# Kernel tuning notes

Measured on AMD Instinct MI355X. Metric: run time of the kernel, lower is better.

The kernel has to match this reference:

```python
import jax, jax.numpy as jnp
import numpy as np

B, SR, D, H, L, NH, ND, E, RK = 64, 29, 768, 3072, 12, 12, 14, 15, 8
S = SR + 1            # cls token + regions
SCALE = 16.0 / 8.0    # lora_alpha / lora_r
NE = L // 2           # number of even (MoE) layers


def _ln(x, g, b, eps):
    m = x.mean(-1, keepdims=True)
    v = ((x - m) ** 2).mean(-1, keepdims=True)
    return (x - m) * jax.lax.rsqrt(v + eps) * g + b


def _ln_plain(x, eps):
    # F.layer_norm with no affine params (expert output norm)
    m = x.mean(-1, keepdims=True)
    v = ((x - m) ** 2).mean(-1, keepdims=True)
    return (x - m) * jax.lax.rsqrt(v + eps)


def _mha(x, Wq, bq, Wk, bk, Wv, bv, Wo, bo):
    b_, s_, _ = x.shape
    dh = D // NH
    q = (x @ Wq.T + bq).reshape(b_, s_, NH, dh)
    k = (x @ Wk.T + bk).reshape(b_, s_, NH, dh)
    v = (x @ Wv.T + bv).reshape(b_, s_, NH, dh)
    att = jax.nn.softmax(jnp.einsum('bqhd,bkhd->bhqk', q, k) / np.float32(np.sqrt(dh)), axis=-1)
    o = jnp.einsum('bhqk,bkhd->bqhd', att, v).reshape(b_, s_, D)
    return o @ Wo.T + bo


def _forward(region_features, mask, cls_token, ln1_g, ln1_b, ln2_g, ln2_b,
             Wq, bq, Wk, bk, Wv, bv, Wao, bao, Wi, bi, Wo, bo, fg, fb,
             cW1, cb1, clng, clnb, cW2, cb2, A_up, B_up, A_down, B_down):
    bsz = region_features.shape[0]
    h = jnp.concatenate([jnp.broadcast_to(cls_token, (bsz, 1, D)), region_features], axis=1)
    col_counts = mask.sum(axis=0)  # [ND], guaranteed > 0 by construction
    for i in range(L):
        n1 = _ln(h, ln1_g[i], ln1_b[i], 1e-12)
        attn = _mha(n1, Wq[i], bq[i], Wk[i], bk[i], Wv[i], bv[i], Wao[i], bao[i])
        res1 = attn + h
        n2 = _ln(res1, ln2_g[i], ln2_b[i], 1e-12)
        inter = jax.nn.gelu(n2 @ Wi[i].T + bi[i], approximate=False)   # [B,S,H]
        base = inter @ Wo[i].T + bo[i]                                  # [B,S,D]
        if i % 2 == 0:
            e = i // 2
            # disease classifier: mask-gather region attention features, mean-pool, per-disease MLP
            region = attn[:, 1:, :]                                     # [B,SR,D]
            pooled = jnp.einsum('rd,brh->bdh', mask, region) / col_counts[None, :, None]
            z = jnp.einsum('bdh,dkh->bdk', pooled, cW1[e]) + cb1[e]
            z = jax.nn.gelu(_ln(z, clng[e], clnb[e], 1e-5), approximate=False)
            preds = jnp.einsum('bdk,dk->bd', z, cW2[e]) + cb2[e]        # [B,ND]
            disease_active = (jax.nn.sigmoid(preds) > 0.5).astype(h.dtype)
            # expert activation: general expert always on; disease experts per region-disease mask
            active = jnp.zeros((bsz, S, E), h.dtype).at[:, :, -1].set(1.0)
            region_active = disease_active[:, None, :] * mask[None, :, :]  # [B,SR,ND]
            active = active.at[:, 1:1 + SR, :ND].set(region_active)
            weights = active / jnp.maximum(active.sum(-1, keepdims=True), 1.0)
            # all 15 LoRA experts densely; zero-weight experts contribute nothing
            lup = jnp.einsum('bser,ehr->bseh', jnp.einsum('bsd,erd->bser', n2, A_up[e]), B_up[e]) * SCALE
            hid = inter[:, :, None, :] + lup                             # [B,S,E,H]
            ldown = jnp.einsum('bser,edr->bsed', jnp.einsum('bseh,erh->bser', hid, A_down[e]), B_down[e]) * SCALE
            out_e = _ln_plain(base[:, :, None, :] + ldown, 1e-5)         # [B,S,E,D]
            ffn_out = jnp.einsum('bsed,bse->bsd', out_e, weights)
        else:
            ffn_out = base
        h = ffn_out + res1
    return _ln(h, fg, fb, 1e-12)


def setup_inputs() -> dict:
    key = jax.random.key(0)
    ks = iter(jax.random.split(key, 64))
    p = lambda *sh: 0.02 * jax.random.normal(next(ks), sh, dtype=jnp.float32)
    g = lambda *sh: 1.0 + 0.02 * jax.random.normal(next(ks), sh, dtype=jnp.float32)
    return dict(
        region_features=jax.random.normal(next(ks), (B, SR, D), dtype=jnp.float32),
        mask=jax.random.bernoulli(next(ks), 0.5, (SR, ND)).astype(jnp.float32).at[0, :].set(1.0),
        cls_token=p(1, 1, D),
        ln1_g=g(L, D), ln1_b=p(L, D), ln2_g=g(L, D), ln2_b=p(L, D),
        Wq=p(L, D, D), bq=p(L, D), Wk=p(L, D, D), bk=p(L, D),
        Wv=p(L, D, D), bv=p(L, D), Wao=p(L, D, D), bao=p(L, D),
        Wi=p(L, H, D), bi=p(L, H), Wo=p(L, D, H), bo=p(L, D),
        fg=g(D), fb=p(D),
        cW1=p(NE, ND, D // 2, D), cb1=p(NE, ND, D // 2),
        clng=g(NE, ND, D // 2), clnb=p(NE, ND, D // 2),
        cW2=p(NE, ND, D // 2), cb2=p(NE, ND),
        A_up=p(NE, E, RK, D), B_up=p(NE, E, H, RK),
        A_down=p(NE, E, RK, H), B_down=p(NE, E, D, RK),
    )


def reference(region_features, mask, cls_token, ln1_g, ln1_b, ln2_g, ln2_b,
              Wq, bq, Wk, bk, Wv, bv, Wao, bao, Wi, bi, Wo, bo, fg, fb,
              cW1, cb1, clng, clnb, cW2, cb2, A_up, B_up, A_down, B_down):
    return _forward(region_features, mask, cls_token, ln1_g, ln1_b, ln2_g, ln2_b,
                    Wq, bq, Wk, bk, Wv, bv, Wao, bao, Wi, bi, Wo, bo, fg, fb,
                    cW1, cb1, clng, clnb, cW2, cb2, A_up, B_up, A_down, B_down)
```

## Files before the change

kernel.cpp:

```cpp
#include <hip/hip_runtime.h>

namespace {

constexpr int kB = 64, kSR = 29, kS = 30, kD = 768, kH = 3072, kL = 12;
constexpr int kNH = 12, kND = 14, kE = 15, kNE = 6;
constexpr int kRows = kB * kS;
constexpr int kQKV = 2304;
constexpr long kPS = (long)kRows * kD;
constexpr long kPSL = (long)kRows * 128;

typedef __attribute__((ext_vector_type(8))) short s16x8;
typedef __attribute__((ext_vector_type(4))) float fx4;

__device__ __forceinline__ float gelu_f(float x) {
  return 0.5f * x * (1.0f + erff(x * 0.70710678118654752f));
}

__device__ __forceinline__ unsigned short f2bf_u(float x) {
  union { float f; unsigned u; } v;
  v.f = x;
  unsigned r = v.u + 0x7fffu + ((v.u >> 16) & 1u);
  return (unsigned short)(r >> 16);
}
__device__ __forceinline__ float bfu2f(unsigned short h) {
  union { unsigned u; float f; } v;
  v.u = ((unsigned)h) << 16;
  return v.f;
}

__device__ __forceinline__ void g2l16(const short* g, short* l) {
  __builtin_amdgcn_global_load_lds(
      (const __attribute__((address_space(1))) unsigned int*)g,
      (__attribute__((address_space(3))) unsigned int*)l, 16, 0, 0);
}

template <int N>
__device__ __forceinline__ void waitcnt_vm() {
  if constexpr (N == 0)
    asm volatile("s_waitcnt vmcnt(0)" ::: "memory");
  else if constexpr (N == 4)
    asm volatile("s_waitcnt vmcnt(4)" ::: "memory");
  else if constexpr (N == 6)
    asm volatile("s_waitcnt vmcnt(6)" ::: "memory");
  else
    asm volatile("s_waitcnt vmcnt(8)" ::: "memory");
  __builtin_amdgcn_sched_barrier(0);
}

__device__ __forceinline__ void swz_block(int& bx, int& by, int& bz) {
  int gx = gridDim.x, gy = gridDim.y;
  int nwg = gx * gy * (int)gridDim.z;
  int orig = blockIdx.x + gx * (blockIdx.y + gy * blockIdx.z);
  int q = nwg >> 3, r = nwg & 7;
  int xcd = orig & 7, idx = orig >> 3;
  int s = (xcd < r ? xcd * (q + 1) : r * (q + 1) + (xcd - r) * q) + idx;
  bx = s % gx;
  int t2 = s / gx;
  by = t2 % gy;
  bz = t2 / gy;
}

__device__ __forceinline__ float block_sum(float v) {
  __shared__ float sb[4];
#pragma unroll
  for (int o = 32; o > 0; o >>= 1) v += __shfl_down(v, o, 64);
  int w = threadIdx.x >> 6;
  __syncthreads();
  if ((threadIdx.x & 63) == 0) sb[w] = v;
  __syncthreads();
  return sb[0] + sb[1] + sb[2] + sb[3];
}

__device__ __forceinline__ float dot8(const float* __restrict__ p,
                                      const float* __restrict__ q) {
  float4 x = *(const float4*)p;
  float4 y = *(const float4*)(p + 4);
  return x.x * q[0] + x.y * q[1] + x.z * q[2] + x.w * q[3] +
         y.x * q[4] + y.y * q[5] + y.z * q[6] + y.w * q[7];
}

template <int BM, int BN, int MODE>
__global__ __launch_bounds__(256) void gemm_hl(
    const short* __restrict__ Ah, const short* __restrict__ Al,
    const short* __restrict__ Bh, const short* __restrict__ Bl,
    const float* __restrict__ bias, float* __restrict__ Cf,
    short* __restrict__ Ch, short* __restrict__ Cl, int K, int ldc, int act,
    int kchunk, long bsA, long bsB, long bsBias, long bsC) {
  constexpr int MFR = BM / 16, NFR = BN / 16;
  constexpr int NA = 2 * MFR, NB = 2 * NFR, LPW = (NA + NB) / 4;
  constexpr int MF_W = MFR / 2, NF_W = NFR / 2;
  constexpr int ABUF = 2 * MFR * 512, BBUF = 2 * NFR * 512;
  __shared__ __align__(16) short As[3][2][MFR][512];
  __shared__ __align__(16) short Bs[3][2][NFR][512];
  int bx, by, bz;
  swz_block(bx, by, bz);
  const int t = threadIdx.x, w = t >> 6, lane = t & 63;
  const int lr = lane & 15, lg = lane >> 4;
  const int m0 = by * BM, n0 = bx * BN;
  const int kst = K >> 5;
  int k0 = 0;
  if (MODE == 1) {
    k0 = bz * kchunk;
    Cf += bz * bsC;
  }
  if (MODE == 2) {
    Ah += bz * bsA;
    Al += bz * bsA;
    Bh += bz * bsB;
    Bl += bz * bsB;
    if (bias) bias += bz * bsBias;
    Cf += bz * bsC;
  }
  const int nsteps = (MODE == 1 ? kchunk : K) >> 5;
  const int wmf = (w & 1) * MF_W, wnf = (w >> 1) * NF_W;

  const short* gp[LPW];
  short* lp[LPW];
  int bo[LPW], adv[LPW];
#pragma unroll
  for (int q = 0; q < LPW; q++) {
    int f = w * LPW + q;
    if (f < NA) {
      int p = f & 1, mf = f >> 1;
      gp[q] = (p ? Al : Ah) + (size_t)(m0 + mf * 16 + lr) * K + k0 + lg * 8;
      lp[q] = &As[0][p][mf][0];
      bo[q] = ABUF;
      adv[q] = 32;
    } else {
      int fb = f - NA, p = fb & 1, nf = fb >> 1;
      gp[q] = (p ? Bl : Bh) + ((size_t)(n0 / 16 + nf) * kst + (k0 >> 5)) * 512 +
              lane * 8;
      lp[q] = &Bs[0][p][nf][0];
      bo[q] = BBUF;
      adv[q] = 512;
    }
  }

  auto stage = [&](int bufidx) {
#pragma unroll
    for (int q = 0; q < LPW; q++) {
      g2l16(gp[q], lp[q] + bufidx * bo[q]);
      gp[q] += adv[q];
    }
  };

  fx4 acc[MF_W][NF_W];
#pragma unroll
  for (int i = 0; i < MF_W; i++)
#pragma unroll
    for (int j = 0; j < NF_W; j++) acc[i][j] = (fx4)0.f;

  stage(0);
  stage(1);
  waitcnt_vm<LPW>();
  __builtin_amdgcn_s_barrier();
  __builtin_amdgcn_sched_barrier(0);

  int cur = 0;
  for (int s = 0; s < nsteps; s++) {
    if (s + 2 < nsteps) {
      int nb = cur + 2;
      if (nb >= 3) nb -= 3;
      stage(nb);
    }
    s16x8 af[MF_W][2], bf[NF_W][2];
#pragma unroll
    for (int fm = 0; fm < MF_W; fm++) {
      af[fm][0] = *(const s16x8*)&As[cur][0][wmf + fm][lane * 8];
      af[fm][1] = *(const s16x8*)&As[cur][1][wmf + fm][lane * 8];
    }
#pragma unroll
    for (int fn = 0; fn < NF_W; fn++) {
      bf[fn][0] = *(const s16x8*)&Bs[cur][0][wnf + fn][lane * 8];
      bf[fn][1] = *(const s16x8*)&Bs[cur][1][wnf + fn][lane * 8];
    }
#pragma unroll
    for (int fm = 0; fm < MF_W; fm++)
#pragma unroll
      for (int fn = 0; fn < NF_W; fn++)
        acc[fm][fn] = __builtin_amdgcn_mfma_f32_16x16x32_bf16(
            af[fm][0], bf[fn][0], acc[fm][fn], 0, 0, 0);
#pragma unroll
    for (int fm = 0; fm < MF_W; fm++)
#pragma unroll
      for (int fn = 0; fn < NF_W; fn++)
        acc[fm][fn] = __builtin_amdgcn_mfma_f32_16x16x32_bf16(
            af[fm][0], bf[fn][1], acc[fm][fn], 0, 0, 0);
#pragma unroll
    for (int fm = 0; fm < MF_W; fm++)
#pragma unroll
      for (int fn = 0; fn < NF_W; fn++)
        acc[fm][fn] = __builtin_amdgcn_mfma_f32_16x16x32_bf16(
            af[fm][1], bf[fn][0], acc[fm][fn], 0, 0, 0);
    if (s + 2 < nsteps)
      waitcnt_vm<LPW>();
    else
      waitcnt_vm<0>();
    __builtin_amdgcn_s_barrier();
    __builtin_amdgcn_sched_barrier(0);
    cur = (cur == 2) ? 0 : cur + 1;
  }

  const int orow = (lane >> 4) * 4;
#pragma unroll
  for (int fm = 0; fm < MF_W; fm++) {
#pragma unroll
    for (int fn = 0; fn < NF_W; fn++) {
      int col = n0 + (wnf + fn) * 16 + lr;
      if (MODE == 1) {
#pragma unroll
        for (int j = 0; j < 4; j++) {
          int row = m0 + (wmf + fm) * 16 + orow + j;
          Cf[(size_t)row * ldc + col] = acc[fm][fn][j];
        }
      } else {
        float bv = bias ? bias[col] : 0.f;
#pragma unroll
        for (int j = 0; j < 4; j++) {
          int row = m0 + (wmf + fm) * 16 + orow + j;
          float v = acc[fm][fn][j] + bv;
          if (act) v = gelu_f(v);
          size_t idx = (size_t)row * ldc + col;
          if (Cf) Cf[idx] = v;
          if (Ch) {
            unsigned short hb = f2bf_u(v);
            Ch[idx] = (short)hb;
            Cl[idx] = (short)f2bf_u(v - bfu2f(hb));
          }
        }
      }
    }
  }
}

__device__ __forceinline__ void pack_store(const float* src, short* ph,
                                           short* pl, size_t o) {
  float4 a = *(const float4*)src;
  float4 b = *(const float4*)(src + 4);
  float v[8] = {a.x, a.y, a.z, a.w, b.x, b.y, b.z, b.w};
  s16x8 hv, lv;
#pragma unroll
  for (int e = 0; e < 8; e++) {
    unsigned short h = f2bf_u(v[e]);
    hv[e] = (short)h;
    lv[e] = (short)f2bf_u(v[e] - bfu2f(h));
  }
  *(s16x8*)(ph + o) = hv;
  *(s16x8*)(pl + o) = lv;
}

__global__ __launch_bounds__(256) void pack_layer_k(
    const float* __restrict__ Wq, const float* __restrict__ Wk,
    const float* __restrict__ Wv, const float* __restrict__ Wao,
    const float* __restrict__ Wi, const float* __restrict__ Wo,
    short* __restrict__ qph, short* __restrict__ qpl, short* __restrict__ aph,
    short* __restrict__ apl, short* __restrict__ iph, short* __restrict__ ipl,
    short* __restrict__ oph, short* __restrict__ opl) {
  int tile = blockIdx.x * 4 + (threadIdx.x >> 6);
  int lane = threadIdx.x & 63;
  int lr = lane & 15, lg = lane >> 4;
  const float* src;
  short *ph, *pl;
  size_t o;
  if (tile < 3456) {
    int nf = tile / 24, ks = tile % 24;
    int row = nf * 16 + lr;
    const float* W = row < 768 ? Wq : row < 1536 ? Wk : Wv;
    int r = row < 768 ? row : row < 1536 ? row - 768 : row - 1536;
    src = W + (size_t)r * 768 + ks * 32 + lg * 8;
    ph = qph; pl = qpl;
    o = (size_t)tile * 512 + lane * 8;
  } else if (tile < 4608) {
    int idx = tile - 3456;
    int nf = idx / 24, ks = idx % 24;
    src = Wao + (size_t)(nf * 16 + lr) * 768 + ks * 32 + lg * 8;
    ph = aph; pl = apl;
    o = (size_t)idx * 512 + lane * 8;
  } else if (tile < 9216) {
    int idx = tile - 4608;
    int nf = idx / 24, ks = idx % 24;
    src = Wi + (size_t)(nf * 16 + lr) * 768 + ks * 32 + lg * 8;
    ph = iph; pl = ipl;
    o = (size_t)idx * 512 + lane * 8;
  } else {
    int idx = tile - 9216;
    int nf = idx / 96, ks = idx % 96;
    src = Wo + (size_t)(nf * 16 + lr) * 3072 + ks * 32 + lg * 8;
    ph = oph; pl = opl;
    o = (size_t)idx * 512 + lane * 8;
  }
  pack_store(src, ph, pl, o);
}

__global__ __launch_bounds__(256) void pack_w_k(const float* __restrict__ W,
                                                short* __restrict__ ph,
                                                short* __restrict__ pl, int K,
                                                int ntiles) {
  int tile = blockIdx.x * 4 + (threadIdx.x >> 6);
  if (tile >= ntiles) return;
  int kst = K >> 5;
  int nf = tile / kst, ks = tile - nf * kst;
  int lane = threadIdx.x & 63;
// ... 80 lines not shown
  for (int c = 0; c < 3; c++) {
    int tt = t + c * 256;
    float dd = (c == 0 ? d0 : c == 1 ? d1 : d2);
    float val = dd * inv * g[tt] + b[tt];
    unsigned short hb = f2bf_u(val);
    yh[rb + tt] = (short)hb;
    yl[rb + tt] = (short)f2bf_u(val - bfu2f(hb));
  }
}

__global__ __launch_bounds__(256) void ln_parts_k(
    const float* __restrict__ parts, const float* __restrict__ b2,
    const float* __restrict__ r2, float* __restrict__ hout,
    const float* __restrict__ g, const float* __restrict__ b,
    short* __restrict__ yh, short* __restrict__ yl, float eps) {
  int row = blockIdx.x;
  int t = threadIdx.x;
  long rb = (long)row * kD;
  float v0, v1, v2;
  {
    float s0 = 0, s1 = 0, s2 = 0;
#pragma unroll
    for (int p = 0; p < 4; p++) {
      s0 += parts[p * kPS + rb + t];
      s1 += parts[p * kPS + rb + t + 256];
      s2 += parts[p * kPS + rb + t + 512];
    }
    v0 = s0 + b2[t] + r2[rb + t];
    v1 = s1 + b2[t + 256] + r2[rb + t + 256];
    v2 = s2 + b2[t + 512] + r2[rb + t + 512];
  }
  hout[rb + t] = v0;
  hout[rb + t + 256] = v1;
  hout[rb + t + 512] = v2;
  float m = block_sum(v0 + v1 + v2) * (1.0f / 768.0f);
  float d0 = v0 - m, d1 = v1 - m, d2 = v2 - m;
  float q = block_sum(d0 * d0 + d1 * d1 + d2 * d2);
  float inv = rsqrtf(q * (1.0f / 768.0f) + eps);
#pragma unroll
  for (int c = 0; c < 3; c++) {
    int tt = t + c * 256;
    float dd = (c == 0 ? d0 : c == 1 ? d1 : d2);
    float val = dd * inv * g[tt] + b[tt];
    unsigned short hb = f2bf_u(val);
    yh[rb + tt] = (short)hb;
    yl[rb + tt] = (short)f2bf_u(val - bfu2f(hb));
  }
}

__global__ __launch_bounds__(256) void ln_row_k(
    const float* __restrict__ parts, const float* __restrict__ b2,
    const float* __restrict__ r2, const float* __restrict__ g,
    const float* __restrict__ b, float* __restrict__ y, float eps) {
  int row = blockIdx.x;
  int t = threadIdx.x;
  long rb = (long)row * kD;
  float s0 = 0, s1 = 0, s2 = 0;
#pragma unroll
  for (int p = 0; p < 4; p++) {
    s0 += parts[p * kPS + rb + t];
    s1 += parts[p * kPS + rb + t + 256];
    s2 += parts[p * kPS + rb + t + 512];
  }
  float v0 = s0 + b2[t] + r2[rb + t];
  float v1 = s1 + b2[t + 256] + r2[rb + t + 256];
  float v2 = s2 + b2[t + 512] + r2[rb + t + 512];
  float m = block_sum(v0 + v1 + v2) * (1.0f / 768.0f);
  float d0 = v0 - m, d1 = v1 - m, d2 = v2 - m;
  float q = block_sum(d0 * d0 + d1 * d1 + d2 * d2);
  float inv = rsqrtf(q * (1.0f / 768.0f) + eps);
  y[rb + t] = d0 * inv * g[t] + b[t];
  y[rb + t + 256] = d1 * inv * g[t + 256] + b[t + 256];
  y[rb + t + 512] = d2 * inv * g[t + 512] + b[t + 512];
}

__global__ __launch_bounds__(256) void addln_bf_k(
    const float* __restrict__ aparts, const float* __restrict__ abias,
    const float* __restrict__ hh, const float* __restrict__ g,
    const float* __restrict__ b, float* __restrict__ r1,
    short* __restrict__ n2h, short* __restrict__ n2l, float eps) {
  int row = blockIdx.x;
  int t = threadIdx.x;
  long rb = (long)row * kD;
  float v0 = aparts[rb + t] + aparts[kPS + rb + t] + abias[t] + hh[rb + t];
  float v1 = aparts[rb + t + 256] + aparts[kPS + rb + t + 256] + abias[t + 256] +
             hh[rb + t + 256];
  float v2 = aparts[rb + t + 512] + aparts[kPS + rb + t + 512] + abias[t + 512] +
             hh[rb + t + 512];
  r1[rb + t] = v0;
  r1[rb + t + 256] = v1;
  r1[rb + t + 512] = v2;
  float m = block_sum(v0 + v1 + v2) * (1.0f / 768.0f);
  float d0 = v0 - m, d1 = v1 - m, d2 = v2 - m;
  float q = block_sum(d0 * d0 + d1 * d1 + d2 * d2);
  float inv = rsqrtf(q * (1.0f / 768.0f) + eps);
#pragma unroll
  for (int c = 0; c < 3; c++) {
    int tt = t + c * 256;
    float dd = (c == 0 ? d0 : c == 1 ? d1 : d2);
    float val = dd * inv * g[tt] + b[tt];
    unsigned short hb = f2bf_u(val);
    n2h[rb + tt] = (short)hb;
    n2l[rb + tt] = (short)f2bf_u(val - bfu2f(hb));
  }
}

__global__ __launch_bounds__(256) void attn_k(const float* __restrict__ qkv,
                                              const float* __restrict__ bq,
                                              const float* __restrict__ bk,
                                              const float* __restrict__ bv,
                                              short* __restrict__ oh,
                                              short* __restrict__ ol) {
  int blk = blockIdx.x;
  int b = blk / kNH, hh = blk % kNH;
  __shared__ float qs[30][65], ks[30][65], vs[30][65], ps[30][32];
  int t = threadIdx.x;
  long ibase = (long)b * kS * kQKV + hh * 64;
  long obase = (long)b * kS * kD + hh * 64;
  for (int idx = t; idx < 1920; idx += 256) {
    int s = idx >> 6, d = idx & 63;
    long a = ibase + (long)s * kQKV + d;
    int bcol = hh * 64 + d;
    qs[s][d] = qkv[a] + bq[bcol];
    ks[s][d] = qkv[a + 768] + bk[bcol];
    vs[s][d] = qkv[a + 1536] + bv[bcol];
  }
  __syncthreads();
  for (int idx = t; idx < 900; idx += 256) {
    int r = idx / 30, c = idx % 30;
    float acc = 0.f;
#pragma unroll
    for (int d = 0; d < 64; d++) acc += qs[r][d] * ks[c][d];
    ps[r][c] = acc * 0.125f;
  }
  __syncthreads();
  if (t < 30) {
    float mx = -1e30f;
#pragma unroll
    for (int c = 0; c < 30; c++) mx = fmaxf(mx, ps[t][c]);
    float sm = 0.f;
#pragma unroll
    for (int c = 0; c < 30; c++) sm += expf(ps[t][c] - mx);
    float inv = 1.0f / sm;
#pragma unroll
    for (int c = 0; c < 30; c++) ps[t][c] = expf(ps[t][c] - mx) * inv;
  }
  __syncthreads();
  for (int idx = t; idx < 1920; idx += 256) {
    int r = idx >> 6, d = idx & 63;
    float acc = 0.f;
#pragma unroll
    for (int c = 0; c < 30; c++) acc += ps[r][c] * vs[c][d];
    long a = obase + (long)r * kD + d;
    unsigned short hb = f2bf_u(acc);
    oh[a] = (short)hb;
    ol[a] = (short)f2bf_u(acc - bfu2f(hb));
  }
}

__global__ __launch_bounds__(256) void pool_k(const float* __restrict__ aparts,
                                              const float* __restrict__ bao,
                                              const float* __restrict__ mask,
                                              const float* __restrict__ cc,
                                              short* __restrict__ ph,
                                              short* __restrict__ pl) {
  int blk = blockIdx.x;
  int d = blk >> 6, b = blk & 63;
  __shared__ float mr[32];
  int t = threadIdx.x;
  if (t < kSR) mr[t] = mask[t * kND + d];
  __syncthreads();
  float inv = 1.0f / cc[d];
  for (int hd = t; hd < kD; hd += 256) {
    float acc = 0.f;
    for (int r = 0; r < kSR; r++) {
      long o = ((long)b * kS + 1 + r) * kD + hd;
      acc += mr[r] * (aparts[o] + aparts[kPS + o]);
    }
    float v = acc * inv + bao[hd];
    unsigned short hb = f2bf_u(v);
    size_t o = (size_t)blk * kD + hd;
    ph[o] = (short)hb;
    pl[o] = (short)f2bf_u(v - bfu2f(hb));
  }
}

__global__ __launch_bounds__(256) void cls2_k(const float* __restrict__ z,
                                              const float* __restrict__ lng,
                                              const float* __restrict__ lnb,
                                              const float* __restrict__ w2,
                                              const float* __restrict__ b2,
                                              float* __restrict__ da) {
  int blk = blockIdx.x;
  int d = blk >> 6, b = blk & 63;
  int t = threadIdx.x;
  const float* zr = z + (long)blk * 384;
  float v0 = zr[t];
  float v1 = (t < 128) ? zr[256 + t] : 0.f;
  float m = block_sum(v0 + v1) * (1.0f / 384.0f);
  float d0 = v0 - m;
  float d1 = (t < 128) ? v1 - m : 0.f;
  float q = block_sum(d0 * d0 + d1 * d1);
  float inv = rsqrtf(q * (1.0f / 384.0f) + 1e-5f);
  const float* lg = lng + (long)d * 384;
  const float* lb = lnb + (long)d * 384;
  const float* wd = w2 + (long)d * 384;
  float p = gelu_f(d0 * inv * lg[t] + lb[t]) * wd[t];
  if (t < 128) p += gelu_f(d1 * inv * lg[256 + t] + lb[256 + t]) * wd[256 + t];
  float ps = block_sum(p);
  if (t == 0) da[b * kND + d] = (ps + b2[d] > 0.f) ? 1.f : 0.f;
}

__global__ __launch_bounds__(256) void vcomb_k(const float* __restrict__ ubp,
                                               const float* __restrict__ iap,
                                               const float* __restrict__ Mm,
                                               float* __restrict__ vv) {
  int idx = blockIdx.x * 256 + threadIdx.x;
  if (idx >= kRows * 120) return;
  int row = idx / 120, c = idx % 120;
  int e = c >> 3, rp = c & 7;
  const float* Me = Mm + e * 64 + rp * 8;
  long rb = (long)row * 128;
  float acc = 0.f;
#pragma unroll
  for (int p = 0; p < 8; p++) acc += iap[p * kPSL + rb + c];
  float uv[8];
#pragma unroll
  for (int r = 0; r < 8; r++) {
    float u = 0.f;
#pragma unroll
    for (int p = 0; p < 4; p++) u += ubp[p * kPSL + rb + e * 8 + r];
    uv[r] = u;
  }
#pragma unroll
  for (int r = 0; r < 8; r++) acc += 2.0f * Me[r] * uv[r];
  vv[rb + c] = acc;
}

__global__ __launch_bounds__(256) void finaleven_k(
    const float* __restrict__ parts, const float* __restrict__ bo,
    const float* __restrict__ res1, const float* __restrict__ vv,
    const float* __restrict__ Bd, const float* __restrict__ da,
    const float* __restrict__ mask, float* __restrict__ h,
    const float* __restrict__ g1, const float* __restrict__ b1,
    short* __restrict__ n1h, short* __restrict__ n1l) {
  int row = blockIdx.x;
  int b = row / kS, s = row % kS;
  int t = threadIdx.x;
  __shared__ float w[16];
  __shared__ float vvs[120];
  if (t < 120) vvs[t] = vv[(long)row * 128 + t];
  if (t < kND) w[t] = (s >= 1) ? da[b * kND + t] * mask[(s - 1) * kND + t] : 0.f;
  if (t == kND) w[kND] = 1.f;
  __syncthreads();
  float wsum = 0.f;
#pragma unroll
  for (int e = 0; e < kE; e++) wsum += w[e];
  float winv = 1.0f / wsum;
  long rb = (long)row * kD;
  float b0 = bo[t], b1v = bo[t + 256], b2v = bo[t + 512];
#pragma unroll
  for (int p = 0; p < 4; p++) {
    b0 += parts[p * kPS + rb + t];
    b1v += parts[p * kPS + rb + t + 256];
    b2v += parts[p * kPS + rb + t + 512];
  }
  float a0 = 0.f, a1 = 0.f, a2 = 0.f;
  for (int e = 0; e < kE; e++) {
    float we = w[e];
    if (we == 0.f) continue;
    const float* vr = vvs + e * 8;
    float y0 = b0 + 2.0f * dot8(Bd + ((long)(e * kD + t)) * 8, vr);
    float y1 = b1v + 2.0f * dot8(Bd + ((long)(e * kD + t + 256)) * 8, vr);
    float y2 = b2v + 2.0f * dot8(Bd + ((long)(e * kD + t + 512)) * 8, vr);
    float m = block_sum(y0 + y1 + y2) * (1.0f / 768.0f);
    float d0 = y0 - m, d1 = y1 - m, d2 = y2 - m;
    float q = block_sum(d0 * d0 + d1 * d1 + d2 * d2);
    float inv = rsqrtf(q * (1.0f / 768.0f) + 1e-5f);
    float sc = we * winv * inv;
    a0 += sc * d0;
    a1 += sc * d1;
    a2 += sc * d2;
  }
  float v0 = a0 + res1[rb + t];
  float v1 = a1 + res1[rb + t + 256];
  float v2 = a2 + res1[rb + t + 512];
  h[rb + t] = v0;
  h[rb + t + 256] = v1;
  h[rb + t + 512] = v2;
  float m = block_sum(v0 + v1 + v2) * (1.0f / 768.0f);
  float d0 = v0 - m, d1 = v1 - m, d2 = v2 - m;
  float q = block_sum(d0 * d0 + d1 * d1 + d2 * d2);
  float inv = rsqrtf(q * (1.0f / 768.0f) + 1e-12f);
#pragma unroll
  for (int c = 0; c < 3; c++) {
    int tt = t + c * 256;
    float dd = (c == 0 ? d0 : c == 1 ? d1 : d2);
    float val = dd * inv * g1[tt] + b1[tt];
    unsigned short hb = f2bf_u(val);
    n1h[rb + tt] = (short)hb;
    n1l[rb + tt] = (short)f2bf_u(val - bfu2f(hb));
  }
}

}

extern "C" void kernel_launch(void* const* d_in, const int* in_sizes, int n_in,
                              void* d_out, int out_size, void* d_ws, size_t ws_size,
                              hipStream_t stream) {
  const float* region = (const float*)d_in[0];
  const float* mask = (const float*)d_in[1];
  const float* cls = (const float*)d_in[2];
  const float* ln1g = (const float*)d_in[3];
  const float* ln1b = (const float*)d_in[4];
  const float* ln2g = (const float*)d_in[5];
  const float* ln2b = (const float*)d_in[6];
  const float* Wq = (const float*)d_in[7];
  const float* bq = (const float*)d_in[8];
  const float* Wk = (const float*)d_in[9];
  const float* bk = (const float*)d_in[10];
  const float* Wv = (const float*)d_in[11];
  const float* bv = (const float*)d_in[12];
  const float* Wao = (const float*)d_in[13];
  const float* bao = (const float*)d_in[14];
  const float* Wi = (const float*)d_in[15];
  const float* bi = (const float*)d_in[16];
  const float* Wo = (const float*)d_in[17];
  const float* bo = (const float*)d_in[18];
  const float* fg = (const float*)d_in[19];
  const float* fb = (const float*)d_in[20];
  const float* cW1 = (const float*)d_in[21];
  const float* cb1 = (const float*)d_in[22];
  const float* clng = (const float*)d_in[23];
  const float* clnb = (const float*)d_in[24];
  const float* cW2 = (const float*)d_in[25];
  const float* cb2 = (const float*)d_in[26];
  const float* Aup = (const float*)d_in[27];
  const float* Bup = (const float*)d_in[28];
  const float* Adn = (const float*)d_in[29];
  const float* Bdn = (const float*)d_in[30];
  float* out = (float*)d_out;

  char* wsb = (char*)d_ws;
  size_t off = 0;
  auto alloc = [&](size_t bytes) {
    char* p = wsb + off;
    off = (off + bytes + 255) & ~(size_t)255;
    return (void*)p;
  };
  float* h = (float*)alloc((size_t)kRows * kD * 4);
  float* qkv = (float*)alloc((size_t)kRows * kQKV * 4);
  float* aop = (float*)alloc((size_t)2 * kRows * kD * 4);
  float* res1 = (float*)alloc((size_t)kRows * kD * 4);
  float* cwop = (float*)alloc((size_t)4 * kRows * kD * 4);
  float* zb = (float*)alloc((size_t)kND * kB * 384 * 4);
  float* da = (float*)alloc((size_t)kB * kND * 4);
  float* ubp = (float*)alloc((size_t)4 * kRows * 128 * 4);
  float* iap = (float*)alloc((size_t)8 * kRows * 128 * 4);
  float* vvb = (float*)alloc((size_t)kRows * 128 * 4);
  float* Mm = (float*)alloc((size_t)kNE * kE * 64 * 4);
  float* cc = (float*)alloc(64);
  short* n1h = (short*)alloc((size_t)kRows * kD * 2);
  short* n1l = (short*)alloc((size_t)kRows * kD * 2);
  short* n2h = (short*)alloc((size_t)kRows * kD * 2);
  short* n2l = (short*)alloc((size_t)kRows * kD * 2);
  short* inth = (short*)alloc((size_t)kRows * kH * 2);
  short* intl = (short*)alloc((size_t)kRows * kH * 2);
  short* pooledh = (short*)alloc((size_t)kND * kB * kD * 2);
  short* pooledl = (short*)alloc((size_t)kND * kB * kD * 2);
  short* qkvph = (short*)alloc((size_t)144 * 24 * 512 * 2);
  short* qkvpl = (short*)alloc((size_t)144 * 24 * 512 * 2);
  short* waoph = (short*)alloc((size_t)48 * 24 * 512 * 2);
  short* waopl = (short*)alloc((size_t)48 * 24 * 512 * 2);
  short* wiph = (short*)alloc((size_t)192 * 24 * 512 * 2);
  short* wipl = (short*)alloc((size_t)192 * 24 * 512 * 2);
  short* woph = (short*)alloc((size_t)48 * 96 * 512 * 2);
  short* wopl = (short*)alloc((size_t)48 * 96 * 512 * 2);
  short* luph = (short*)alloc((size_t)8 * 24 * 512 * 2);
  short* lupl = (short*)alloc((size_t)8 * 24 * 512 * 2);
  short* ldph = (short*)alloc((size_t)8 * 96 * 512 * 2);
  short* ldpl = (short*)alloc((size_t)8 * 96 * 512 * 2);
  short* cw1ph = (short*)alloc((size_t)336 * 24 * 512 * 2);
  short* cw1pl = (short*)alloc((size_t)336 * 24 * 512 * 2);

  concat_k<<<(kRows * kD + 255) / 256, 256, 0, stream>>>(region, cls, h);
  cc_k<<<1, 32, 0, stream>>>(mask, cc);
  mmat_k<<<kNE * kE, 256, 0, stream>>>(Adn, Bup, Mm);

  const int nDD = kD * kD;
  const int nDH = kD * kH;

  ln_bf_k<<<kRows, 256, 0, stream>>>(h, ln1g, ln1b, n1h, n1l, 1e-12f);

  for (int i = 0; i < kL; i++) {
    int le = i >> 1;
    bool even = (i % 2) == 0;
    pack_layer_k<<<3456, 256, 0, stream>>>(
        Wq + (long)i * nDD, Wk + (long)i * nDD, Wv + (long)i * nDD,
        Wao + (long)i * nDD, Wi + (long)i * nDH, Wo + (long)i * nDH, qkvph,
        qkvpl, waoph, waopl, wiph, wipl, woph, wopl);

    gemm_hl<128, 128, 0><<<dim3(18, 15), 256, 0, stream>>>(
        n1h, n1l, qkvph, qkvpl, nullptr, qkv, nullptr, nullptr, 768, kQKV, 0, 0,
        0, 0, 0, 0);
    attn_k<<<kB * kNH, 256, 0, stream>>>(qkv, bq + i * kD, bk + i * kD,
                                         bv + i * kD, n1h, n1l);
    gemm_hl<128, 128, 1><<<dim3(6, 15, 2), 256, 0, stream>>>(
        n1h, n1l, waoph, waopl, nullptr, aop, nullptr, nullptr, 768, kD, 0, 384,
        0, 0, 0, kPS);
    addln_bf_k<<<kRows, 256, 0, stream>>>(aop, bao + i * kD, h, ln2g + i * kD,
                                          ln2b + i * kD, res1, n2h, n2l, 1e-12f);
    gemm_hl<128, 128, 0><<<dim3(24, 15), 256, 0, stream>>>(
        n2h, n2l, wiph, wipl, bi + i * kH, nullptr, inth, intl, 768, kH, 1, 0,
        0, 0, 0, 0);
    gemm_hl<128, 128, 1><<<dim3(6, 15, 4), 256, 0, stream>>>(
        inth, intl, woph, wopl, nullptr, cwop, nullptr, nullptr, 3072, kD, 0,
        768, 0, 0, 0, kPS);
    if (even) {
      pack_pad_k<<<48, 256, 0, stream>>>(Aup + (long)le * kE * 8 * kD, luph,
                                         lupl, 768);
      pack_pad_k<<<192, 256, 0, stream>>>(Adn + (long)le * kE * 8 * kH, ldph,
                                          ldpl, 3072);
      pack_w_k<<<(336 * 24) / 4, 256, 0, stream>>>(
          cW1 + (long)le * kND * 384 * kD, cw1ph, cw1pl, 768, 336 * 24);
      gemm_hl<128, 128, 1><<<dim3(1, 15, 4), 256, 0, stream>>>(
          n2h, n2l, luph, lupl, nullptr, ubp, nullptr, nullptr, 768, 128, 0, 192,
          0, 0, 0, kPSL);
      gemm_hl<128, 128, 1><<<dim3(1, 15, 8), 256, 0, stream>>>(
          inth, intl, ldph, ldpl, nullptr, iap, nullptr, nullptr, 3072, 128, 0,
          384, 0, 0, 0, kPSL);
      pool_k<<<kND * kB, 256, 0, stream>>>(aop, bao + i * kD, mask, cc, pooledh,
                                           pooledl);
      gemm_hl<64, 64, 2><<<dim3(6, 1, 14), 256, 0, stream>>>(
          pooledh, pooledl, cw1ph, cw1pl, cb1 + (long)le * kND * 384, zb,
          nullptr, nullptr, 768, 384, 0, 0, (long)64 * kD, (long)576 * 512, 384,
          (long)64 * 384);
      cls2_k<<<kND * kB, 256, 0, stream>>>(zb, clng + (long)le * kND * 384,
                                           clnb + (long)le * kND * 384,
                                           cW2 + (long)le * kND * 384,
                                           cb2 + le * kND, da);
      vcomb_k<<<(kRows * 120 + 255) / 256, 256, 0, stream>>>(
          ubp, iap, Mm + le * kE * 64, vvb);
      finaleven_k<<<kRows, 256, 0, stream>>>(
          cwop, bo + i * kD, res1, vvb, Bdn + (long)le * kE * kD * 8, da, mask,
          h, ln1g + (i + 1) * kD, ln1b + (i + 1) * kD, n1h, n1l);
    } else if (i < kL - 1) {
      ln_parts_k<<<kRows, 256, 0, stream>>>(cwop, bo + i * kD, res1, h,
                                            ln1g + (i + 1) * kD,
                                            ln1b + (i + 1) * kD, n1h, n1l,
                                            1e-12f);
    } else {
      ln_row_k<<<kRows, 256, 0, stream>>>(cwop, bo + i * kD, res1, fg, fb, out,
                                          1e-12f);
    }
  }
}
```

Before: 3.269 ms.

## Replace LDS-staged GEMM with register double-buffered direct-global GEMM

The triple-buffered LDS pipeline (global_load_lds plus barriers) is replaced by a kernel where each wave loads its own 64x64 tile fragments straight from global memory into registers, ping-ponging two register sets. This removes LDS traffic and block-wide barriers. In exchange, operands that waves could share through LDS are now fetched separately, raising global/L2 traffic and register pressure. The classifier GEMM grid is halved and rows beyond M are skipped.

```diff
diff --git a/kernel.cpp b/kernel.cpp
--- a/kernel.cpp
+++ b/kernel.cpp
@@ -26,25 +26,6 @@
   union { unsigned u; float f; } v;
   v.u = ((unsigned)h) << 16;
   return v.f;
-}
-
-__device__ __forceinline__ void g2l16(const short* g, short* l) {
-  __builtin_amdgcn_global_load_lds(
-      (const __attribute__((address_space(1))) unsigned int*)g,
-      (__attribute__((address_space(3))) unsigned int*)l, 16, 0, 0);
-}
-
-template <int N>
-__device__ __forceinline__ void waitcnt_vm() {
-  if constexpr (N == 0)
-    asm volatile("s_waitcnt vmcnt(0)" ::: "memory");
-  else if constexpr (N == 4)
-    asm volatile("s_waitcnt vmcnt(4)" ::: "memory");
-  else if constexpr (N == 6)
-    asm volatile("s_waitcnt vmcnt(6)" ::: "memory");
-  else
-    asm volatile("s_waitcnt vmcnt(8)" ::: "memory");
-  __builtin_amdgcn_sched_barrier(0);
 }
 
 __device__ __forceinline__ void swz_block(int& bx, int& by, int& bz) {
@@ -79,24 +60,17 @@
          y.x * q[4] + y.y * q[5] + y.z * q[6] + y.w * q[7];
 }
 
-template <int BM, int BN, int MODE>
-__global__ __launch_bounds__(256) void gemm_hl(
+template <int MODE>
+__global__ __launch_bounds__(256) void gemm_reg(
     const short* __restrict__ Ah, const short* __restrict__ Al,
     const short* __restrict__ Bh, const short* __restrict__ Bl,
     const float* __restrict__ bias, float* __restrict__ Cf,
     short* __restrict__ Ch, short* __restrict__ Cl, int K, int ldc, int act,
-    int kchunk, long bsA, long bsB, long bsBias, long bsC) {
-  constexpr int MFR = BM / 16, NFR = BN / 16;
-  constexpr int NA = 2 * MFR, NB = 2 * NFR, LPW = (NA + NB) / 4;
-  constexpr int MF_W = MFR / 2, NF_W = NFR / 2;
-  constexpr int ABUF = 2 * MFR * 512, BBUF = 2 * NFR * 512;
-  __shared__ __align__(16) short As[3][2][MFR][512];
-  __shared__ __align__(16) short Bs[3][2][NFR][512];
+    int kchunk, long bsA, long bsB, long bsBias, long bsC, int M) {
   int bx, by, bz;
   swz_block(bx, by, bz);
   const int t = threadIdx.x, w = t >> 6, lane = t & 63;
   const int lr = lane & 15, lg = lane >> 4;
-  const int m0 = by * BM, n0 = bx * BN;
   const int kst = K >> 5;
   int k0 = 0;
   if (MODE == 1) {
@@ -111,113 +85,112 @@
     if (bias) bias += bz * bsBias;
     Cf += bz * bsC;
   }
+  const int m0 = by * 128 + (w & 1) * 64;
+  const int n0 = bx * 128 + (w >> 1) * 64;
+  if (MODE == 2 && m0 >= M) return;
   const int nsteps = (MODE == 1 ? kchunk : K) >> 5;
-  const int wmf = (w & 1) * MF_W, wnf = (w >> 1) * NF_W;
-
-  const short* gp[LPW];
-  short* lp[LPW];
-  int bo[LPW], adv[LPW];
-#pragma unroll
-  for (int q = 0; q < LPW; q++) {
-    int f = w * LPW + q;
-    if (f < NA) {
-      int p = f & 1, mf = f >> 1;
-      gp[q] = (p ? Al : Ah) + (size_t)(m0 + mf * 16 + lr) * K + k0 + lg * 8;
-      lp[q] = &As[0][p][mf][0];
-      bo[q] = ABUF;
-      adv[q] = 32;
-    } else {
-      int fb = f - NA, p = fb & 1, nf = fb >> 1;
-      gp[q] = (p ? Bl : Bh) + ((size_t)(n0 / 16 + nf) * kst + (k0 >> 5)) * 512 +
-              lane * 8;
-      lp[q] = &Bs[0][p][nf][0];
-      bo[q] = BBUF;
-      adv[q] = 512;
+
+  const short* ga[4][2];
+  const short* gb[4][2];
+#pragma unroll
+  for (int mf = 0; mf < 4; mf++) {
+    size_t ro = (size_t)(m0 + mf * 16 + lr) * K + k0 + lg * 8;
+    ga[mf][0] = Ah + ro;
+    ga[mf][1] = Al + ro;
+  }
+#pragma unroll
+  for (int nf = 0; nf < 4; nf++) {
+    size_t to = ((size_t)(n0 / 16 + nf) * kst + (k0 >> 5)) * 512 + lane * 8;
+    gb[nf][0] = Bh + to;
+    gb[nf][1] = Bl + to;
+  }
+
+  fx4 acc[4][4];
+#pragma unroll
+  for (int i = 0; i < 4; i++)
+#pragma unroll
+    for (int j = 0; j < 4; j++) acc[i][j] = (fx4)0.f;
+
+  s16x8 a0[4][2], b0[4][2], a1[4][2], b1[4][2];
+
+  auto load0 = [&]() {
+#pragma unroll
+    for (int mf = 0; mf < 4; mf++) {
+      a0[mf][0] = *(const s16x8*)ga[mf][0];
+      a0[mf][1] = *(const s16x8*)ga[mf][1];
+      ga[mf][0] += 32;
+      ga[mf][1] += 32;
     }
-  }
-
-  auto stage = [&](int bufidx) {
-#pragma unroll
-    for (int q = 0; q < LPW; q++) {
-      g2l16(gp[q], lp[q] + bufidx * bo[q]);
-      gp[q] += adv[q];
+#pragma unroll
+    for (int nf = 0; nf < 4; nf++) {
+      b0[nf][0] = *(const s16x8*)gb[nf][0];
+      b0[nf][1] = *(const s16x8*)gb[nf][1];
+      gb[nf][0] += 512;
+      gb[nf][1] += 512;
     }
   };
-
-  fx4 acc[MF_W][NF_W];
-#pragma unroll
-  for (int i = 0; i < MF_W; i++)
-#pragma unroll
-    for (int j = 0; j < NF_W; j++) acc[i][j] = (fx4)0.f;
-
-  stage(0);
-  stage(1);
-  waitcnt_vm<LPW>();
-  __builtin_amdgcn_s_barrier();
-  __builtin_amdgcn_sched_barrier(0);
-
-  int cur = 0;
-  for (int s = 0; s < nsteps; s++) {
-    if (s + 2 < nsteps) {
-      int nb = cur + 2;
-      if (nb >= 3) nb -= 3;
-      stage(nb);
+  auto load1 = [&]() {
+#pragma unroll
+    for (int mf = 0; mf < 4; mf++) {
+      a1[mf][0] = *(const s16x8*)ga[mf][0];
+      a1[mf][1] = *(const s16x8*)ga[mf][1];
+      ga[mf][0] += 32;
+      ga[mf][1] += 32;
     }
-    s16x8 af[MF_W][2], bf[NF_W][2];
-#pragma unroll
-    for (int fm = 0; fm < MF_W; fm++) {
-      af[fm][0] = *(const s16x8*)&As[cur][0][wmf + fm][lane * 8];
-      af[fm][1] = *(const s16x8*)&As[cur][1][wmf + fm][lane * 8];
+#pragma unroll
+    for (int nf = 0; nf < 4; nf++) {
+      b1[nf][0] = *(const s16x8*)gb[nf][0];
+      b1[nf][1] = *(const s16x8*)gb[nf][1];
+      gb[nf][0] += 512;
+      gb[nf][1] += 512;
     }
-#pragma unroll
-    for (int fn = 0; fn < NF_W; fn++) {
-      bf[fn][0] = *(const s16x8*)&Bs[cur][0][wnf + fn][lane * 8];
-      bf[fn][1] = *(const s16x8*)&Bs[cur][1][wnf + fn][lane * 8];
-    }
-#pragma unroll
-    for (int fm = 0; fm < MF_W; fm++)
-#pragma unroll
-      for (int fn = 0; fn < NF_W; fn++)
+  };
+  auto mfma3 = [&](s16x8 (&a)[4][2], s16x8 (&b)[4][2]) {
+#pragma unroll
+    for (int fm = 0; fm < 4; fm++)
+#pragma unroll
+      for (int fn = 0; fn < 4; fn++)
         acc[fm][fn] = __builtin_amdgcn_mfma_f32_16x16x32_bf16(
-            af[fm][0], bf[fn][0], acc[fm][fn], 0, 0, 0);
-#pragma unroll
-    for (int fm = 0; fm < MF_W; fm++)
-#pragma unroll
-      for (int fn = 0; fn < NF_W; fn++)
+            a[fm][0], b[fn][0], acc[fm][fn], 0, 0, 0);
+#pragma unroll
+    for (int fm = 0; fm < 4; fm++)
+#pragma unroll
+      for (int fn = 0; fn < 4; fn++)
         acc[fm][fn] = __builtin_amdgcn_mfma_f32_16x16x32_bf16(
-            af[fm][0], bf[fn][1], acc[fm][fn], 0, 0, 0);
-#pragma unroll
-    for (int fm = 0; fm < MF_W; fm++)
-#pragma unroll
-      for (int fn = 0; fn < NF_W; fn++)
+            a[fm][0], b[fn][1], acc[fm][fn], 0, 0, 0);
+#pragma unroll
+    for (int fm = 0; fm < 4; fm++)
+#pragma unroll
+      for (int fn = 0; fn < 4; fn++)
         acc[fm][fn] = __builtin_amdgcn_mfma_f32_16x16x32_bf16(
-            af[fm][1], bf[fn][0], acc[fm][fn], 0, 0, 0);
-    if (s + 2 < nsteps)
-      waitcnt_vm<LPW>();
-    else
-      waitcnt_vm<0>();
-    __builtin_amdgcn_s_barrier();
-    __builtin_amdgcn_sched_barrier(0);
-    cur = (cur == 2) ? 0 : cur + 1;
+            a[fm][1], b[fn][0], acc[fm][fn], 0, 0, 0);
+  };
+
+  load0();
+  for (int s = 0; s < nsteps; s += 2) {
+    load1();
+    mfma3(a0, b0);
+    if (s + 2 < nsteps) load0();
+    mfma3(a1, b1);
   }
 
   const int orow = (lane >> 4) * 4;
 #pragma unroll
-  for (int fm = 0; fm < MF_W; fm++) {
-#pragma unroll
-    for (int fn = 0; fn < NF_W; fn++) {
-      int col = n0 + (wnf + fn) * 16 + lr;
+  for (int fm = 0; fm < 4; fm++) {
+#pragma unroll
+    for (int fn = 0; fn < 4; fn++) {
+      int col = n0 + fn * 16 + lr;
       if (MODE == 1) {
 #pragma unroll
         for (int j = 0; j < 4; j++) {
-          int row = m0 + (wmf + fm) * 16 + orow + j;
+          int row = m0 + fm * 16 + orow + j;
           Cf[(size_t)row * ldc + col] = acc[fm][fn][j];
         }
       } else {
         float bv = bias ? bias[col] : 0.f;
 #pragma unroll
         for (int j = 0; j < 4; j++) {
-          int row = m0 + (wmf + fm) * 16 + orow + j;
+          int row = m0 + fm * 16 + orow + j;
           float v = acc[fm][fn][j] + bv;
           if (act) v = gelu_f(v);
           size_t idx = (size_t)row * ldc + col;
@@ -782,22 +755,22 @@
         Wao + (long)i * nDD, Wi + (long)i * nDH, Wo + (long)i * nDH, qkvph,
         qkvpl, waoph, waopl, wiph, wipl, woph, wopl);
 
-    gemm_hl<128, 128, 0><<<dim3(18, 15), 256, 0, stream>>>(
+    gemm_reg<0><<<dim3(18, 15), 256, 0, stream>>>(
         n1h, n1l, qkvph, qkvpl, nullptr, qkv, nullptr, nullptr, 768, kQKV, 0, 0,
-        0, 0, 0, 0);
+        0, 0, 0, 0, 0);
     attn_k<<<kB * kNH, 256, 0, stream>>>(qkv, bq + i * kD, bk + i * kD,
                                          bv + i * kD, n1h, n1l);
-    gemm_hl<128, 128, 1><<<dim3(6, 15, 2), 256, 0, stream>>>(
+    gemm_reg<1><<<dim3(6, 15, 2), 256, 0, stream>>>(
         n1h, n1l, waoph, waopl, nullptr, aop, nullptr, nullptr, 768, kD, 0, 384,
-        0, 0, 0, kPS);
+        0, 0, 0, kPS, 0);
     addln_bf_k<<<kRows, 256, 0, stream>>>(aop, bao + i * kD, h, ln2g + i * kD,
                                           ln2b + i * kD, res1, n2h, n2l, 1e-12f);
-    gemm_hl<128, 128, 0><<<dim3(24, 15), 256, 0, stream>>>(
+    gemm_reg<0><<<dim3(24, 15), 256, 0, stream>>>(
         n2h, n2l, wiph, wipl, bi + i * kH, nullptr, inth, intl, 768, kH, 1, 0,
-        0, 0, 0, 0);
-    gemm_hl<128, 128, 1><<<dim3(6, 15, 4), 256, 0, stream>>>(
+        0, 0, 0, 0, 0);
+    gemm_reg<1><<<dim3(6, 15, 4), 256, 0, stream>>>(
         inth, intl, woph, wopl, nullptr, cwop, nullptr, nullptr, 3072, kD, 0,
-        768, 0, 0, 0, kPS);
+        768, 0, 0, 0, kPS, 0);
     if (even) {
       pack_pad_k<<<48, 256, 0, stream>>>(Aup + (long)le * kE * 8 * kD, luph,
                                          lupl, 768);
@@ -805,18 +778,18 @@
                                           ldpl, 3072);
       pack_w_k<<<(336 * 24) / 4, 256, 0, stream>>>(
           cW1 + (long)le * kND * 384 * kD, cw1ph, cw1pl, 768, 336 * 24);
-      gemm_hl<128, 128, 1><<<dim3(1, 15, 4), 256, 0, stream>>>(
+      gemm_reg<1><<<dim3(1, 15, 4), 256, 0, stream>>>(
           n2h, n2l, luph, lupl, nullptr, ubp, nullptr, nullptr, 768, 128, 0, 192,
-          0, 0, 0, kPSL);
-      gemm_hl<128, 128, 1><<<dim3(1, 15, 8), 256, 0, stream>>>(
+          0, 0, 0, kPSL, 0);
+      gemm_reg<1><<<dim3(1, 15, 8), 256, 0, stream>>>(
           inth, intl, ldph, ldpl, nullptr, iap, nullptr, nullptr, 3072, 128, 0,
-          384, 0, 0, 0, kPSL);
+          384, 0, 0, 0, kPSL, 0);
       pool_k<<<kND * kB, 256, 0, stream>>>(aop, bao + i * kD, mask, cc, pooledh,
                                            pooledl);
-      gemm_hl<64, 64, 2><<<dim3(6, 1, 14), 256, 0, stream>>>(
+      gemm_reg<2><<<dim3(3, 1, 14), 256, 0, stream>>>(
           pooledh, pooledl, cw1ph, cw1pl, cb1 + (long)le * kND * 384, zb,
           nullptr, nullptr, 768, 384, 0, 0, (long)64 * kD, (long)576 * 512, 384,
-          (long)64 * 384);
+          (long)64 * 384, 64);
       cls2_k<<<kND * kB, 256, 0, stream>>>(zb, clng + (long)le * kND * 384,
                                            clnb + (long)le * kND * 384,
                                            cW2 + (long)le * kND * 384,
```

After: 4.070 ms. 24.5% more time.

## Fuse LoRA up/down projections into FFN GEMMs and retile GEMMs to 128x64

Applied to the files above, without the earlier changes.

On MoE layers, the LoRA up and down projection weights are packed as extra column tiles appended to the Wi and Wo packed buffers. The FFN GEMMs now emit those extra columns into separate output buffers through a new column-split epilogue, which removes two small separate GEMM launches. All main GEMMs switch from 128x128 to 128x64 tiles with more grid blocks, and the QKV and attention-output GEMMs use split-K partials (2 and 3 partials) that attention, add-LN and pooling now sum. This trades more partial-sum traffic and reduction work for higher occupancy and fewer launches.

```diff
diff --git a/kernel.cpp b/kernel.cpp
--- a/kernel.cpp
+++ b/kernel.cpp
@@ -8,6 +8,8 @@
 constexpr int kQKV = 2304;
 constexpr long kPS = (long)kRows * kD;
 constexpr long kPSL = (long)kRows * 128;
+constexpr long kQS = (long)kRows * kQKV;
+constexpr int kBIG = 1 << 30;
 
 typedef __attribute__((ext_vector_type(8))) short s16x8;
 typedef __attribute__((ext_vector_type(4))) float fx4;
@@ -84,8 +86,9 @@
     const short* __restrict__ Ah, const short* __restrict__ Al,
     const short* __restrict__ Bh, const short* __restrict__ Bl,
     const float* __restrict__ bias, float* __restrict__ Cf,
-    short* __restrict__ Ch, short* __restrict__ Cl, int K, int ldc, int act,
-    int kchunk, long bsA, long bsB, long bsBias, long bsC) {
+    short* __restrict__ Ch, short* __restrict__ Cl, float* __restrict__ C2,
+    int K, int ldc, int ldc2, int act, int kchunk, int nsplit, long bsA,
+    long bsB, long bsBias, long bsC, long bsC2) {
   constexpr int MFR = BM / 16, NFR = BN / 16;
   constexpr int NA = 2 * MFR, NB = 2 * NFR, LPW = (NA + NB) / 4;
   constexpr int MF_W = MFR / 2, NF_W = NFR / 2;
@@ -102,6 +105,7 @@
   if (MODE == 1) {
     k0 = bz * kchunk;
     Cf += bz * bsC;
+    C2 += bz * bsC2;
   }
   if (MODE == 2) {
     Ah += bz * bsA;
@@ -202,16 +206,33 @@
   }
 
   const int orow = (lane >> 4) * 4;
+  const bool rg2 = (n0 >= nsplit);
 #pragma unroll
   for (int fm = 0; fm < MF_W; fm++) {
 #pragma unroll
     for (int fn = 0; fn < NF_W; fn++) {
       int col = n0 + (wnf + fn) * 16 + lr;
       if (MODE == 1) {
+        if (rg2) {
+          int c2 = col - nsplit;
+#pragma unroll
+          for (int j = 0; j < 4; j++) {
+            int row = m0 + (wmf + fm) * 16 + orow + j;
+            C2[(size_t)row * ldc2 + c2] = acc[fm][fn][j];
+          }
+        } else {
+#pragma unroll
+          for (int j = 0; j < 4; j++) {
+            int row = m0 + (wmf + fm) * 16 + orow + j;
+            Cf[(size_t)row * ldc + col] = acc[fm][fn][j];
+          }
+        }
+      } else if (rg2) {
+        int c2 = col - nsplit;
 #pragma unroll
         for (int j = 0; j < 4; j++) {
           int row = m0 + (wmf + fm) * 16 + orow + j;
-          Cf[(size_t)row * ldc + col] = acc[fm][fn][j];
+          C2[(size_t)row * ldc2 + c2] = acc[fm][fn][j];
         }
       } else {
         float bv = bias ? bias[col] : 0.f;
@@ -464,11 +485,16 @@
   int row = blockIdx.x;
   int t = threadIdx.x;
   long rb = (long)row * kD;
-  float v0 = aparts[rb + t] + aparts[kPS + rb + t] + abias[t] + hh[rb + t];
-  float v1 = aparts[rb + t + 256] + aparts[kPS + rb + t + 256] + abias[t + 256] +
-             hh[rb + t + 256];
-  float v2 = aparts[rb + t + 512] + aparts[kPS + rb + t + 512] + abias[t + 512] +
-             hh[rb + t + 512];
+  float s0 = 0, s1 = 0, s2 = 0;
+#pragma unroll
+  for (int p = 0; p < 3; p++) {
+    s0 += aparts[p * kPS + rb + t];
+    s1 += aparts[p * kPS + rb + t + 256];
+    s2 += aparts[p * kPS + rb + t + 512];
+  }
+  float v0 = s0 + abias[t] + hh[rb + t];
+  float v1 = s1 + abias[t + 256] + hh[rb + t + 256];
+  float v2 = s2 + abias[t + 512] + hh[rb + t + 512];
   r1[rb + t] = v0;
   r1[rb + t + 256] = v1;
   r1[rb + t + 512] = v2;
@@ -503,9 +529,9 @@
     int s = idx >> 6, d = idx & 63;
     long a = ibase + (long)s * kQKV + d;
     int bcol = hh * 64 + d;
-    qs[s][d] = qkv[a] + bq[bcol];
-    ks[s][d] = qkv[a + 768] + bk[bcol];
-    vs[s][d] = qkv[a + 1536] + bv[bcol];
+    qs[s][d] = qkv[a] + qkv[kQS + a] + bq[bcol];
+    ks[s][d] = qkv[a + 768] + qkv[kQS + a + 768] + bk[bcol];
+    vs[s][d] = qkv[a + 1536] + qkv[kQS + a + 1536] + bv[bcol];
   }
   __syncthreads();
   for (int idx = t; idx < 900; idx += 256) {
@@ -557,7 +583,7 @@
     float acc = 0.f;
     for (int r = 0; r < kSR; r++) {
       long o = ((long)b * kS + 1 + r) * kD + hd;
-      acc += mr[r] * (aparts[o] + aparts[kPS + o]);
+      acc += mr[r] * (aparts[o] + aparts[kPS + o] + aparts[2 * kPS + o]);
     }
     float v = acc * inv + bao[hd];
     unsigned short hb = f2bf_u(v);
@@ -593,7 +619,7 @@
   if (t == 0) da[b * kND + d] = (ps + b2[d] > 0.f) ? 1.f : 0.f;
 }
 
-__global__ __launch_bounds__(256) void vcomb_k(const float* __restrict__ ubp,
+__global__ __launch_bounds__(256) void vcomb_k(const float* __restrict__ ub,
                                                const float* __restrict__ iap,
                                                const float* __restrict__ Mm,
                                                float* __restrict__ vv) {
@@ -605,17 +631,10 @@
   long rb = (long)row * 128;
   float acc = 0.f;
 #pragma unroll
-  for (int p = 0; p < 8; p++) acc += iap[p * kPSL + rb + c];
-  float uv[8];
-#pragma unroll
-  for (int r = 0; r < 8; r++) {
-    float u = 0.f;
-#pragma unroll
-    for (int p = 0; p < 4; p++) u += ubp[p * kPSL + rb + e * 8 + r];
-    uv[r] = u;
-  }
-#pragma unroll
-  for (int r = 0; r < 8; r++) acc += 2.0f * Me[r] * uv[r];
+  for (int p = 0; p < 4; p++) acc += iap[p * kPSL + rb + c];
+  const float* ur = ub + rb + e * 8;
+#pragma unroll
+  for (int r = 0; r < 8; r++) acc += 2.0f * Me[r] * ur[r];
   vv[rb + c] = acc;
 }
 
@@ -731,14 +750,14 @@
     return (void*)p;
   };
   float* h = (float*)alloc((size_t)kRows * kD * 4);
-  float* qkv = (float*)alloc((size_t)kRows * kQKV * 4);
-  float* aop = (float*)alloc((size_t)2 * kRows * kD * 4);
+  float* qkvp = (float*)alloc((size_t)2 * kRows * kQKV * 4);
+  float* aop = (float*)alloc((size_t)3 * kRows * kD * 4);
   float* res1 = (float*)alloc((size_t)kRows * kD * 4);
   float* cwop = (float*)alloc((size_t)4 * kRows * kD * 4);
   float* zb = (float*)alloc((size_t)kND * kB * 384 * 4);
   float* da = (float*)alloc((size_t)kB * kND * 4);
-  float* ubp = (float*)alloc((size_t)4 * kRows * 128 * 4);
-  float* iap = (float*)alloc((size_t)8 * kRows * 128 * 4);
+  float* ub = (float*)alloc((size_t)kRows * 128 * 4);
+  float* iap = (float*)alloc((size_t)4 * kRows * 128 * 4);
   float* vvb = (float*)alloc((size_t)kRows * 128 * 4);
   float* Mm = (float*)alloc((size_t)kNE * kE * 64 * 4);
   float* cc = (float*)alloc(64);
@@ -754,16 +773,16 @@
   short* qkvpl = (short*)alloc((size_t)144 * 24 * 512 * 2);
   short* waoph = (short*)alloc((size_t)48 * 24 * 512 * 2);
   short* waopl = (short*)alloc((size_t)48 * 24 * 512 * 2);
-  short* wiph = (short*)alloc((size_t)192 * 24 * 512 * 2);
-  short* wipl = (short*)alloc((size_t)192 * 24 * 512 * 2);
-  short* woph = (short*)alloc((size_t)48 * 96 * 512 * 2);
-  short* wopl = (short*)alloc((size_t)48 * 96 * 512 * 2);
-  short* luph = (short*)alloc((size_t)8 * 24 * 512 * 2);
-  short* lupl = (short*)alloc((size_t)8 * 24 * 512 * 2);
-  short* ldph = (short*)alloc((size_t)8 * 96 * 512 * 2);
-  short* ldpl = (short*)alloc((size_t)8 * 96 * 512 * 2);
+  short* wiph = (short*)alloc((size_t)200 * 24 * 512 * 2);
+  short* wipl = (short*)alloc((size_t)200 * 24 * 512 * 2);
+  short* woph = (short*)alloc((size_t)56 * 96 * 512 * 2);
+  short* wopl = (short*)alloc((size_t)56 * 96 * 512 * 2);
   short* cw1ph = (short*)alloc((size_t)336 * 24 * 512 * 2);
   short* cw1pl = (short*)alloc((size_t)336 * 24 * 512 * 2);
+  short* luph = wiph + (size_t)192 * 24 * 512;
+  short* lupl = wipl + (size_t)192 * 24 * 512;
+  short* ldph = woph + (size_t)48 * 96 * 512;
+  short* ldpl = wopl + (size_t)48 * 96 * 512;
 
   concat_k<<<(kRows * kD + 255) / 256, 256, 0, stream>>>(region, cls, h);
   cc_k<<<1, 32, 0, stream>>>(mask, cc);
@@ -781,23 +800,6 @@
         Wq + (long)i * nDD, Wk + (long)i * nDD, Wv + (long)i * nDD,
         Wao + (long)i * nDD, Wi + (long)i * nDH, Wo + (long)i * nDH, qkvph,
         qkvpl, waoph, waopl, wiph, wipl, woph, wopl);
-
-    gemm_hl<128, 128, 0><<<dim3(18, 15), 256, 0, stream>>>(
-        n1h, n1l, qkvph, qkvpl, nullptr, qkv, nullptr, nullptr, 768, kQKV, 0, 0,
-        0, 0, 0, 0);
-    attn_k<<<kB * kNH, 256, 0, stream>>>(qkv, bq + i * kD, bk + i * kD,
-                                         bv + i * kD, n1h, n1l);
-    gemm_hl<128, 128, 1><<<dim3(6, 15, 2), 256, 0, stream>>>(
-        n1h, n1l, waoph, waopl, nullptr, aop, nullptr, nullptr, 768, kD, 0, 384,
-        0, 0, 0, kPS);
-    addln_bf_k<<<kRows, 256, 0, stream>>>(aop, bao + i * kD, h, ln2g + i * kD,
-                                          ln2b + i * kD, res1, n2h, n2l, 1e-12f);
-    gemm_hl<128, 128, 0><<<dim3(24, 15), 256, 0, stream>>>(
-        n2h, n2l, wiph, wipl, bi + i * kH, nullptr, inth, intl, 768, kH, 1, 0,
-        0, 0, 0, 0);
-    gemm_hl<128, 128, 1><<<dim3(6, 15, 4), 256, 0, stream>>>(
-        inth, intl, woph, wopl, nullptr, cwop, nullptr, nullptr, 3072, kD, 0,
-        768, 0, 0, 0, kPS);
     if (even) {
       pack_pad_k<<<48, 256, 0, stream>>>(Aup + (long)le * kE * 8 * kD, luph,
                                          lupl, 768);
@@ -805,24 +807,37 @@
                                           ldpl, 3072);
       pack_w_k<<<(336 * 24) / 4, 256, 0, stream>>>(
           cW1 + (long)le * kND * 384 * kD, cw1ph, cw1pl, 768, 336 * 24);
-      gemm_hl<128, 128, 1><<<dim3(1, 15, 4), 256, 0, stream>>>(
-          n2h, n2l, luph, lupl, nullptr, ubp, nullptr, nullptr, 768, 128, 0, 192,
-          0, 0, 0, kPSL);
-      gemm_hl<128, 128, 1><<<dim3(1, 15, 8), 256, 0, stream>>>(
-          inth, intl, ldph, ldpl, nullptr, iap, nullptr, nullptr, 3072, 128, 0,
-          384, 0, 0, 0, kPSL);
+    }
+
+    gemm_hl<128, 64, 1><<<dim3(36, 15, 2), 256, 0, stream>>>(
+        n1h, n1l, qkvph, qkvpl, nullptr, qkvp, nullptr, nullptr, nullptr, 768,
+        kQKV, 0, 0, 384, kBIG, 0, 0, 0, kQS, 0);
+    attn_k<<<kB * kNH, 256, 0, stream>>>(qkvp, bq + i * kD, bk + i * kD,
+                                         bv + i * kD, n1h, n1l);
+    gemm_hl<128, 64, 1><<<dim3(12, 15, 3), 256, 0, stream>>>(
+        n1h, n1l, waoph, waopl, nullptr, aop, nullptr, nullptr, nullptr, 768,
+        kD, 0, 0, 256, kBIG, 0, 0, 0, kPS, 0);
+    addln_bf_k<<<kRows, 256, 0, stream>>>(aop, bao + i * kD, h, ln2g + i * kD,
+                                          ln2b + i * kD, res1, n2h, n2l, 1e-12f);
+    gemm_hl<128, 64, 0><<<dim3(even ? 50 : 48, 15), 256, 0, stream>>>(
+        n2h, n2l, wiph, wipl, bi + i * kH, nullptr, inth, intl, ub, 768, kH,
+        128, 1, 0, even ? 3072 : kBIG, 0, 0, 0, 0, 0);
+    gemm_hl<128, 64, 1><<<dim3(even ? 14 : 12, 15, 4), 256, 0, stream>>>(
+        inth, intl, woph, wopl, nullptr, cwop, nullptr, nullptr, iap, 3072, kD,
+        128, 0, 768, even ? 768 : kBIG, 0, 0, 0, kPS, kPSL);
+    if (even) {
       pool_k<<<kND * kB, 256, 0, stream>>>(aop, bao + i * kD, mask, cc, pooledh,
                                            pooledl);
       gemm_hl<64, 64, 2><<<dim3(6, 1, 14), 256, 0, stream>>>(
           pooledh, pooledl, cw1ph, cw1pl, cb1 + (long)le * kND * 384, zb,
-          nullptr, nullptr, 768, 384, 0, 0, (long)64 * kD, (long)576 * 512, 384,
-          (long)64 * 384);
+          nullptr, nullptr, nullptr, 768, 384, 0, 0, 0, kBIG, (long)64 * kD,
+          (long)576 * 512, 384, (long)64 * 384, 0);
       cls2_k<<<kND * kB, 256, 0, stream>>>(zb, clng + (long)le * kND * 384,
                                            clnb + (long)le * kND * 384,
                                            cW2 + (long)le * kND * 384,
                                            cb2 + le * kND, da);
       vcomb_k<<<(kRows * 120 + 255) / 256, 256, 0, stream>>>(
-          ubp, iap, Mm + le * kE * 64, vvb);
+          ub, iap, Mm + le * kE * 64, vvb);
       finaleven_k<<<kRows, 256, 0, stream>>>(
           cwop, bo + i * kD, res1, vvb, Bdn + (long)le * kE * kD * 8, da, mask,
           h, ln1g + (i + 1) * kD, ln1b + (i + 1) * kD, n1h, n1l);
```

Result: faster. 3.059 ms (-6.4%).
